# Kernel optimization log

Measured on AMD Instinct MI355X. Metric: run time of the kernel, lower is better.

## Reference

```python
import jax, jax.numpy as jnp
import numpy as np

N = 50000      # nodes
E = 800000     # edges
F = 128        # num_features
H = 128        # hidden_channels
L = 3          # num_layers
P = 32         # num_partitions
EPS = 1e-5     # BatchNorm1d eps


def _batchnorm(h):
    # BatchNorm1d(affine=False, track_running_stats=False): batch stats, biased var
    m = jnp.mean(h, axis=0)
    v = jnp.var(h, axis=0)
    return (h - m) * jax.lax.rsqrt(v + EPS)


def setup_inputs() -> dict:
    key = jax.random.key(0)
    ks = jax.random.split(key, 12)
    x = jax.random.normal(ks[0], (N, F), dtype=jnp.float32)
    edge_index = jax.random.randint(ks[1], (2, E), 0, N)
    edge_weights = jax.random.uniform(ks[2], (E,), dtype=jnp.float32)
    partitions = (jax.random.uniform(ks[3], (N, P)) < (1.0 / P)).astype(jnp.float32)
    node_weights = jax.random.uniform(ks[4], (N,), dtype=jnp.float32)
    edge_curr_node = jax.random.uniform(ks[5], (N,), dtype=jnp.float32)
    conv_w = 0.05 * jax.random.normal(ks[6], (L, F, H), dtype=jnp.float32)
    conv_b = jnp.zeros((L, H), dtype=jnp.float32)
    lin1_w = 0.05 * jax.random.normal(ks[7], (4 * H, H), dtype=jnp.float32)
    lin1_b = jnp.zeros((H,), dtype=jnp.float32)
    lin2_w = 0.05 * jax.random.normal(ks[8], (H, 1), dtype=jnp.float32)
    lin2_b = jnp.zeros((1,), dtype=jnp.float32)
    return {"x": x, "edge_index": edge_index, "edge_weights": edge_weights,
            "partitions": partitions, "node_weights": node_weights,
            "edge_curr_node": edge_curr_node, "conv_w": conv_w, "conv_b": conv_b,
            "lin1_w": lin1_w, "lin1_b": lin1_b, "lin2_w": lin2_w,
            "lin2_b": lin2_b, "curr_node_id": 123}


def reference(x, edge_index, edge_weights, partitions, node_weights,
              edge_curr_node, conv_w, conv_b, lin1_w, lin1_b, lin2_w, lin2_b,
              curr_node_id):
    src, dst = edge_index[0], edge_index[1]
    # GCN normalization with added self-loops (weight 1)
    deg = jax.ops.segment_sum(edge_weights, dst, num_segments=N) + 1.0
    dinv = jax.lax.rsqrt(deg)
    norm = dinv[src] * edge_weights * dinv[dst]          # [E]
    self_norm = (dinv * dinv)[:, None]                   # [N,1]

    h = x
    for l in range(L):
        hw = h @ conv_w[l] + conv_b[l]                   # [N,H]
        agg = jax.ops.segment_sum(hw[src] * norm[:, None], dst, num_segments=N)
        agg = agg + hw * self_norm                       # self-loop term
        h = jax.nn.relu(_batchnorm(agg))

    x_curr = h[curr_node_id]                             # [H]
    # mlp scoring: concat [h | x_curr | edge_col repeated to 2H] -> [N,4H]
    cat = jnp.concatenate([
        h,
        jnp.broadcast_to(x_curr[None, :], (N, H)),
        jnp.broadcast_to(edge_curr_node[:, None], (N, 2 * H)),
    ], axis=1)
    scores = jax.nn.relu(cat @ lin1_w + lin1_b) @ lin2_w + lin2_b  # [N,1]
    # pool == 'sum'
    partition_scores = scores.T @ partitions             # [1,P]
    return (partition_scores, h)
```

## Files before the change

### kernel.cpp

```cpp
#include <hip/hip_runtime.h>

#define N_NODES 50000
#define N_EDGES 800000
#define NP 50048
#define MAXDEG 64
#define PADK 136
#define NCOPY 64
#define EB 3125
#define WPB 512

typedef __bf16 bf16_8 __attribute__((ext_vector_type(8)));
typedef float  f32_4  __attribute__((ext_vector_type(4)));

__device__ inline float2 bf2f2(unsigned int u) {
    union { unsigned int i; float f; } a, b;
    a.i = u << 16;
    b.i = u & 0xffff0000u;
    return make_float2(a.f, b.f);
}

__global__ void k_init_wprep(int* __restrict__ fillp, float* __restrict__ colpart,
                             float* __restrict__ out_head,
                             const float* __restrict__ conv_w, const float* __restrict__ lin1_w,
                             __bf16* __restrict__ WT, float* __restrict__ svec) {
    int b = blockIdx.x;
    if (b < EB) {
        int i = b * 256 + threadIdx.x;
        fillp[i] = 0;
        if (i < 2 * NCOPY * 128) colpart[i] = 0.f;
        if (i < 32) out_head[i] = 0.f;
    } else if (b < EB + WPB) {
        int b2 = b - EB;
        int mat = b2 >> 7, n = b2 & 127, k = threadIdx.x;
        if (k < 128) {
            const float* srcm = (mat < 3) ? (conv_w + (size_t)mat * 16384) : lin1_w;
            WT[((size_t)mat * 128 + n) * 128 + k] = (__bf16)srcm[(size_t)k * 128 + n];
        }
    } else {
        int j = threadIdx.x;
        if (j < 128) {
            float s = 0.f;
            for (int k = 256; k < 512; ++k) s += lin1_w[(size_t)k * 128 + j];
            svec[j] = s;
        }
    }
}

__global__ void k_fillover(const int* __restrict__ src, const int* __restrict__ dst,
                           const float* __restrict__ ew,
                           int* __restrict__ fillp, uint2* __restrict__ esn) {
    int e = blockIdx.x * 256 + threadIdx.x;
    if (e >= N_EDGES) return;
    int d = dst[e];
    int pos = atomicAdd(&fillp[d * 16], 1);
    if (pos < MAXDEG)
        esn[(size_t)d * MAXDEG + pos] = make_uint2((unsigned)src[e], __float_as_uint(ew[e]));
}

__global__ void k_node(const uint2* __restrict__ esn, const int* __restrict__ fillp,
                       float* __restrict__ dinv) {
    int n = blockIdx.x * 256 + threadIdx.x;
    if (n >= N_NODES) return;
    int c = min(fillp[n * 16], MAXDEG);
    float s = 1.0f;
    for (int i = 0; i < c; ++i) s += __uint_as_float(esn[(size_t)n * MAXDEG + i].y);
    dinv[n] = rsqrtf(s);
}

template <int AMODE>
__global__ __launch_bounds__(256) void k_gemm_mfma(const float* __restrict__ A,
                                                   const float* __restrict__ mean,
                                                   const float* __restrict__ rstd,
                                                   const __bf16* __restrict__ WT,
                                                   const float* __restrict__ bias,
                                                   __bf16* __restrict__ C, int nrows) {
    __shared__ __bf16 As[64 * PADK];
    __shared__ __bf16 Ws[128 * PADK];
    int t = threadIdx.x;
    int rowBase = blockIdx.x * 64;
    const uint4* WTg = (const uint4*)WT;
    for (int i = t; i < 2048; i += 256) {
        int n = i >> 4, k8 = i & 15;
        *(uint4*)&Ws[n * PADK + k8 * 8] = WTg[i];
    }
    const float4* A4 = (const float4*)A;
    const float4* M4 = (const float4*)mean;
    const float4* R4 = (const float4*)rstd;
    for (int i = t; i < 1024; i += 256) {
        int r = i >> 4, k8 = i & 15;
        int gr = rowBase + r;
        float4 a0 = make_float4(0.f, 0.f, 0.f, 0.f), a1 = a0;
        if (gr < nrows) {
            a0 = A4[(size_t)gr * 32 + k8 * 2];
            a1 = A4[(size_t)gr * 32 + k8 * 2 + 1];
        }
        if (AMODE == 1) {
            float4 m0 = M4[k8 * 2], m1 = M4[k8 * 2 + 1];
            float4 r0 = R4[k8 * 2], r1 = R4[k8 * 2 + 1];
            a0.x = fmaxf((a0.x - m0.x) * r0.x, 0.f); a0.y = fmaxf((a0.y - m0.y) * r0.y, 0.f);
            a0.z = fmaxf((a0.z - m0.z) * r0.z, 0.f); a0.w = fmaxf((a0.w - m0.w) * r0.w, 0.f);
            a1.x = fmaxf((a1.x - m1.x) * r1.x, 0.f); a1.y = fmaxf((a1.y - m1.y) * r1.y, 0.f);
            a1.z = fmaxf((a1.z - m1.z) * r1.z, 0.f); a1.w = fmaxf((a1.w - m1.w) * r1.w, 0.f);
        }
        bf16_8 o = { (__bf16)a0.x, (__bf16)a0.y, (__bf16)a0.z, (__bf16)a0.w,
                     (__bf16)a1.x, (__bf16)a1.y, (__bf16)a1.z, (__bf16)a1.w };
        *(bf16_8*)&As[r * PADK + k8 * 8] = o;
    }
    __syncthreads();
    int wave = t >> 6, lane = t & 63, quad = lane >> 4, m = lane & 15;
    int ar = wave * 16 + m;
    f32_4 acc[8];
#pragma unroll
    for (int i = 0; i < 8; ++i) acc[i] = (f32_4){0.f, 0.f, 0.f, 0.f};
#pragma unroll
    for (int kk = 0; kk < 4; ++kk) {
        bf16_8 a = *(const bf16_8*)&As[ar * PADK + kk * 32 + quad * 8];
#pragma unroll
        for (int n0 = 0; n0 < 8; ++n0) {
            bf16_8 b = *(const bf16_8*)&Ws[(n0 * 16 + m) * PADK + kk * 32 + quad * 8];
            acc[n0] = __builtin_amdgcn_mfma_f32_16x16x32_bf16(a, b, acc[n0], 0, 0, 0);
        }
    }
    __syncthreads();
#pragma unroll
    for (int n0 = 0; n0 < 8; ++n0) {
        int col = n0 * 16 + m;
        float bi = bias[col];
#pragma unroll
        for (int r = 0; r < 4; ++r) {
            int rr = wave * 16 + quad * 4 + r;
            As[rr * PADK + col] = (__bf16)(acc[n0][r] + bi);
        }
    }
    __syncthreads();
    uint4* Cg = (uint4*)C;
    for (int i = t; i < 1024; i += 256) {
        int r = i >> 4, k8 = i & 15;
        int gr = rowBase + r;
        if (gr < nrows) Cg[(size_t)gr * 16 + k8] = *(const uint4*)&As[r * PADK + k8 * 8];
    }
}

__global__ __launch_bounds__(256) void k_agg(const __bf16* __restrict__ hwb,
                                             const uint2* __restrict__ esn,
                                             const int* __restrict__ fillp,
                                             const float* __restrict__ dinv,
                                             float* __restrict__ agg,
                                             float* __restrict__ colpart) {
    __shared__ float red1[4 * 128], red2[4 * 128];
    int t = threadIdx.x;
    int n = (blockIdx.x * 256 + t) >> 6;
    int lane = t & 63, wave = t >> 6;
    float2 acc = make_float2(0.f, 0.f);
    const unsigned int* hw32 = (const unsigned int*)hwb;
    if (n < N_NODES) {
        float dvn = dinv[n];
        float2 sv = bf2f2(hw32[(size_t)n * 64 + lane]);
        acc.x = sv.x * dvn * dvn; acc.y = sv.y * dvn * dvn;
        int num = min(fillp[n * 16], MAXDEG);
        int s_l = 0; float w_l = 0.f;
        if (lane < num) {
            uint2 e = esn[(size_t)n * MAXDEG + lane];
            s_l = (int)e.x;
            w_l = dinv[s_l] * __uint_as_float(e.y) * dvn;
        }
        int i = 0;
        for (; i + 8 <= num; i += 8) {
            int ss[8]; float ww[8]; unsigned uu[8];
#pragma unroll
            for (int j = 0; j < 8; ++j) { ss[j] = __shfl(s_l, i + j); ww[j] = __shfl(w_l, i + j); }
#pragma unroll
            for (int j = 0; j < 8; ++j) uu[j] = hw32[(size_t)ss[j] * 64 + lane];
#pragma unroll
            for (int j = 0; j < 8; ++j) {
                float2 f = bf2f2(uu[j]);
                acc.x += f.x * ww[j]; acc.y += f.y * ww[j];
            }
        }
        for (; i < num; ++i) {
            int s = __shfl(s_l, i);
            float w = __shfl(w_l, i);
            float2 f = bf2f2(hw32[(size_t)s * 64 + lane]);
            acc.x += f.x * w; acc.y += f.y * w;
        }
        ((float2*)agg)[(size_t)n * 64 + lane] = acc;
    }
    *(float2*)&red1[wave * 128 + 2 * lane] = acc;
    *(float2*)&red2[wave * 128 + 2 * lane] = make_float2(acc.x * acc.x, acc.y * acc.y);
    __syncthreads();
    if (t < 128) {
        float s = red1[t] + red1[128 + t] + red1[256 + t] + red1[384 + t];
        float q = red2[t] + red2[128 + t] + red2[256 + t] + red2[384 + t];
        int c = blockIdx.x & (NCOPY - 1);
        unsafeAtomicAdd(&colpart[c * 128 + t], s);
        unsafeAtomicAdd(&colpart[NCOPY * 128 + c * 128 + t], q);
    }
}

__global__ void k_bnfinal(float* colpart, float* mean, float* rstd) {
    int j = threadIdx.x;
    float s = 0.f, q = 0.f;
    for (int c = 0; c < NCOPY; ++c) {
        s += colpart[c * 128 + j];
        q += colpart[NCOPY * 128 + c * 128 + j];
        colpart[c * 128 + j] = 0.f;
        colpart[NCOPY * 128 + c * 128 + j] = 0.f;
    }
    float m = s * (1.0f / N_NODES);
    float v = q * (1.0f / N_NODES) - m * m;
    mean[j] = m;
    rstd[j] = rsqrtf(v + 1e-5f);
}

__global__ void k_prep(const float* __restrict__ agg, const float* __restrict__ mean,
                       const float* __restrict__ rstd, const int* __restrict__ cid,
                       const float* __restrict__ lin1w, const float* __restrict__ lin1b,
                       float* c0) {
    __shared__ float xc[128];
    int t = threadIdx.x;
    int cn = cid[0];
    float a = agg[(size_t)cn * 128 + t];
    xc[t] = fmaxf((a - mean[t]) * rstd[t], 0.f);
    __syncthreads();
    float acc = lin1b[t];
    for (int k = 0; k < 128; ++k)
        acc += xc[k] * lin1w[(size_t)(128 + k) * 128 + t];
    c0[t] = acc;
}

__global__ __launch_bounds__(256) void k_score_mfma(const float* __restrict__ agg,
                                                    const float* __restrict__ mean,
                                                    const float* __restrict__ rstd,
                                                    const __bf16* __restrict__ WT,
                                                    const float* __restrict__ c0,
                                                    const float* __restrict__ svec,
                                                    const float* __restrict__ ecn,
                                                    const float* __restrict__ lin2w,
                                                    const float* __restrict__ lin2b,
                                                    float* __restrict__ scores,
                                                    float* __restrict__ hout,
                                                    int nrows) {
    __shared__ __bf16 As[64 * PADK];
    __shared__ __bf16 Ws[128 * PADK];
    __shared__ float c0s[128], svs[128], l2s[128];
    int t = threadIdx.x;
    int rowBase = blockIdx.x * 64;
    const uint4* WTg = (const uint4*)WT;
    for (int i = t; i < 2048; i += 256) {
        int n = i >> 4, k8 = i & 15;
        *(uint4*)&Ws[n * PADK + k8 * 8] = WTg[i];
    }
    const float4* A4 = (const float4*)agg;
    const float4* M4 = (const float4*)mean;
    const float4* R4 = (const float4*)rstd;
    float4* H4 = (float4*)hout;
    for (int i = t; i < 1024; i += 256) {
        int r = i >> 4, k8 = i & 15;
        int gr = rowBase + r;
        float4 a0 = make_float4(0.f, 0.f, 0.f, 0.f), a1 = a0;
        if (gr < nrows) {
            a0 = A4[(size_t)gr * 32 + k8 * 2];
            a1 = A4[(size_t)gr * 32 + k8 * 2 + 1];
        }
        float4 m0 = M4[k8 * 2], m1 = M4[k8 * 2 + 1];
        float4 r0 = R4[k8 * 2], r1 = R4[k8 * 2 + 1];
        float4 f0, f1;
        f0.x = fmaxf((a0.x - m0.x) * r0.x, 0.f); f0.y = fmaxf((a0.y - m0.y) * r0.y, 0.f);
        f0.z = fmaxf((a0.z - m0.z) * r0.z, 0.f); f0.w = fmaxf((a0.w - m0.w) * r0.w, 0.f);
        f1.x = fmaxf((a1.x - m1.x) * r1.x, 0.f); f1.y = fmaxf((a1.y - m1.y) * r1.y, 0.f);
        f1.z = fmaxf((a1.z - m1.z) * r1.z, 0.f); f1.w = fmaxf((a1.w - m1.w) * r1.w, 0.f);
        if (gr < nrows) {
            H4[(size_t)gr * 32 + k8 * 2] = f0;
            H4[(size_t)gr * 32 + k8 * 2 + 1] = f1;
        }
        bf16_8 o = { (__bf16)f0.x, (__bf16)f0.y, (__bf16)f0.z, (__bf16)f0.w,
                     (__bf16)f1.x, (__bf16)f1.y, (__bf16)f1.z, (__bf16)f1.w };
        *(bf16_8*)&As[r * PADK + k8 * 8] = o;
    }
    if (t < 128) { c0s[t] = c0[t]; svs[t] = svec[t]; l2s[t] = lin2w[t]; }
    __syncthreads();
    int wave = t >> 6, lane = t & 63, quad = lane >> 4, m = lane & 15;
    int ar = wave * 16 + m;
    f32_4 acc[8];
#pragma unroll
    for (int i = 0; i < 8; ++i) acc[i] = (f32_4){0.f, 0.f, 0.f, 0.f};
#pragma unroll
    for (int kk = 0; kk < 4; ++kk) {
        bf16_8 a = *(const bf16_8*)&As[ar * PADK + kk * 32 + quad * 8];
#pragma unroll
        for (int n0 = 0; n0 < 8; ++n0) {
            bf16_8 b = *(const bf16_8*)&Ws[(n0 * 16 + m) * PADK + kk * 32 + quad * 8];
            acc[n0] = __builtin_amdgcn_mfma_f32_16x16x32_bf16(a, b, acc[n0], 0, 0, 0);
        }
    }
    float l2b = lin2b[0];
#pragma unroll
    for (int r = 0; r < 4; ++r) {
        int row = rowBase + wave * 16 + quad * 4 + r;
        float e = (row < nrows) ? ecn[row] : 0.f;
        float partial = 0.f;
#pragma unroll
        for (int n0 = 0; n0 < 8; ++n0) {
            int col = n0 * 16 + m;
            float v = acc[n0][r] + c0s[col] + e * svs[col];
            partial += fmaxf(v, 0.f) * l2s[col];
        }
        partial += __shfl_xor(partial, 8, 16);
        partial += __shfl_xor(partial, 4, 16);
        partial += __shfl_xor(partial, 2, 16);
        partial += __shfl_xor(partial, 1, 16);
        if (m == 0 && row < nrows) scores[row] = partial + l2b;
    }
}

__global__ void k_partition(const float* __restrict__ scores, const float* __restrict__ part,
                            float* out) {
    __shared__ float red[256];
    int t = threadIdx.x;
    int p = t & 31, rg = t >> 5;
    float acc = 0.f;
    for (int r = blockIdx.x * 8 + rg; r < N_NODES; r += gridDim.x * 8)
        acc += scores[r] * part[(size_t)r * 32 + p];
    red[t] = acc;
    __syncthreads();
    if (t < 32) {
        float s = 0.f;
        for (int i = 0; i < 8; ++i) s += red[i * 32 + t];
        unsafeAtomicAdd(&out[t], s);
    }
}

extern "C" void kernel_launch(void* const* d_in, const int* in_sizes, int n_in,
                              void* d_out, int out_size, void* d_ws, size_t ws_size,
                              hipStream_t stream) {
    const float* x        = (const float*)d_in[0];
    const int*   eidx     = (const int*)d_in[1];
    const float* ew       = (const float*)d_in[2];
    const float* parts    = (const float*)d_in[3];
    const float* ecn      = (const float*)d_in[5];
    const float* conv_w   = (const float*)d_in[6];
    const float* conv_b   = (const float*)d_in[7];
    const float* lin1_w   = (const float*)d_in[8];
    const float* lin1_b   = (const float*)d_in[9];
    const float* lin2_w   = (const float*)d_in[10];
    const float* lin2_b   = (const float*)d_in[11];
    const int*   cid      = (const int*)d_in[12];

    const int* src = eidx;
    const int* dst = eidx + N_EDGES;

    char* p = (char*)d_ws;
    auto alloc = [&](size_t bytes) { char* r = p; p += (bytes + 255) & ~size_t(255); return r; };
    int*    fillp   = (int*)alloc((size_t)N_NODES * 16 * 4);
    uint2*  esn     = (uint2*)alloc((size_t)N_NODES * MAXDEG * 8);
    float*  dinv    = (float*)alloc(NP * 4);
    float*  scores  = (float*)alloc(NP * 4);
    float*  colpart = (float*)alloc(2 * NCOPY * 128 * 4);
    float*  mean    = (float*)alloc(128 * 4);
    float*  rstd    = (float*)alloc(128 * 4);
    float*  c0      = (float*)alloc(128 * 4);
    float*  svec    = (float*)alloc(128 * 4);
    __bf16* WT      = (__bf16*)alloc(4 * 128 * 128 * 2);
    __bf16* hwb     = (__bf16*)alloc((size_t)N_NODES * 128 * 2);
    float*  agg     = (float*)alloc((size_t)N_NODES * 128 * 4);

    float* out_head = (float*)d_out;
    float* hbuf     = (float*)d_out + 32;

    const int NB = (NP + 255) / 256;
    const int GB = (N_NODES + 63) / 64;
    const int AB = (N_NODES * 64 + 255) / 256;

    k_init_wprep<<<EB + WPB + 1, 256, 0, stream>>>(fillp, colpart, out_head,
                                                   conv_w, lin1_w, WT, svec);
    k_fillover<<<EB, 256, 0, stream>>>(src, dst, ew, fillp, esn);
    k_node<<<NB, 256, 0, stream>>>(esn, fillp, dinv);

    for (int l = 0; l < 3; ++l) {
        if (l == 0)
            k_gemm_mfma<0><<<GB, 256, 0, stream>>>(x, mean, rstd, WT, conv_b, hwb, N_NODES);
        else
            k_gemm_mfma<1><<<GB, 256, 0, stream>>>(agg, mean, rstd, WT + (size_t)l * 16384,
                                                   conv_b + (size_t)l * 128, hwb, N_NODES);
        k_agg<<<AB, 256, 0, stream>>>(hwb, esn, fillp, dinv, agg, colpart);
        k_bnfinal<<<1, 128, 0, stream>>>(colpart, mean, rstd);
    }

    k_prep<<<1, 128, 0, stream>>>(agg, mean, rstd, cid, lin1_w, lin1_b, c0);
    k_score_mfma<<<GB, 256, 0, stream>>>(agg, mean, rstd, WT + (size_t)3 * 16384, c0, svec,
                                         ecn, lin2_w, lin2_b, scores, hbuf, N_NODES);
    k_partition<<<256, 256, 0, stream>>>(scores, parts, out_head);
}
```

Measured before the change: 354.2 us.

## Build compact CSR adjacency via bucketed counting sort instead of padded atomic fill

Replaces the padded per-node edge slots (fixed MAXDEG, one global atomic per edge) with a two-level counting sort: a per-block histogram over 64 destination buckets, a scan, a scatter into bucket order, then a per-bucket kernel that builds an exact CSR in shared memory and computes dinv there. The aggregation kernel now reads contiguous CSR ranges, folds dinv[dst] into the stored weight, handles any degree in chunks of 64 rather than truncating at 64, and unrolls the gather by 16. The aim is to cut global atomic contention and the memory footprint of the padded layout, and to improve gather ILP, at the cost of several extra small launches and an extra pass over the edges.

Measured after the change: 460.0 us. +29.9%, slower.

```diff
diff --git a/kernel.cpp b/kernel.cpp
--- a/kernel.cpp
+++ b/kernel.cpp
@@ -3,10 +3,11 @@
 #define N_NODES 50000
 #define N_EDGES 800000
 #define NP 50048
-#define MAXDEG 64
+#define BKT 784
+#define NBKT 64
+#define HB 782
 #define PADK 136
 #define NCOPY 64
-#define EB 3125
 #define WPB 512
 
 typedef __bf16 bf16_8 __attribute__((ext_vector_type(8)));
@@ -19,18 +20,16 @@
     return make_float2(a.f, b.f);
 }
 
-__global__ void k_init_wprep(int* __restrict__ fillp, float* __restrict__ colpart,
-                             float* __restrict__ out_head,
+__global__ void k_init_wprep(float* __restrict__ colpart, float* __restrict__ out_head,
                              const float* __restrict__ conv_w, const float* __restrict__ lin1_w,
                              __bf16* __restrict__ WT, float* __restrict__ svec) {
     int b = blockIdx.x;
-    if (b < EB) {
+    if (b < 64) {
         int i = b * 256 + threadIdx.x;
-        fillp[i] = 0;
-        if (i < 2 * NCOPY * 128) colpart[i] = 0.f;
+        colpart[i] = 0.f;
         if (i < 32) out_head[i] = 0.f;
-    } else if (b < EB + WPB) {
-        int b2 = b - EB;
+    } else if (b < 64 + WPB) {
+        int b2 = b - 64;
         int mat = b2 >> 7, n = b2 & 127, k = threadIdx.x;
         if (k < 128) {
             const float* srcm = (mat < 3) ? (conv_w + (size_t)mat * 16384) : lin1_w;
@@ -46,25 +45,123 @@
     }
 }
 
-__global__ void k_fillover(const int* __restrict__ src, const int* __restrict__ dst,
-                           const float* __restrict__ ew,
-                           int* __restrict__ fillp, uint2* __restrict__ esn) {
-    int e = blockIdx.x * 256 + threadIdx.x;
-    if (e >= N_EDGES) return;
-    int d = dst[e];
-    int pos = atomicAdd(&fillp[d * 16], 1);
-    if (pos < MAXDEG)
-        esn[(size_t)d * MAXDEG + pos] = make_uint2((unsigned)src[e], __float_as_uint(ew[e]));
-}
-
-__global__ void k_node(const uint2* __restrict__ esn, const int* __restrict__ fillp,
-                       float* __restrict__ dinv) {
-    int n = blockIdx.x * 256 + threadIdx.x;
-    if (n >= N_NODES) return;
-    int c = min(fillp[n * 16], MAXDEG);
-    float s = 1.0f;
-    for (int i = 0; i < c; ++i) s += __uint_as_float(esn[(size_t)n * MAXDEG + i].y);
-    dinv[n] = rsqrtf(s);
+__global__ void k_hist(const int* __restrict__ dst, int* __restrict__ counts) {
+    __shared__ int c[NBKT];
+    int t = threadIdx.x, b = blockIdx.x;
+    if (t < NBKT) c[t] = 0;
+    __syncthreads();
+    int e0 = b * 1024;
+    for (int i = t; i < 1024; i += 256) {
+        int e = e0 + i;
+        if (e < N_EDGES) atomicAdd(&c[dst[e] / BKT], 1);
+    }
+    __syncthreads();
+    if (t < NBKT) counts[t * HB + b] = c[t];
+}
+
+__global__ void k_scan(int* __restrict__ counts, int* __restrict__ bucketStart) {
+    __shared__ int p[256];
+    int t = threadIdx.x;
+    int base = t * 196;
+    int sum = 0;
+    for (int i = 0; i < 196; ++i) {
+        int f = base + i;
+        if (f < NBKT * HB) sum += counts[f];
+    }
+    p[t] = sum;
+    __syncthreads();
+    int own = sum;
+    for (int d = 1; d < 256; d <<= 1) {
+        int v = (t >= d) ? p[t - d] : 0;
+        __syncthreads();
+        p[t] += v;
+        __syncthreads();
+    }
+    int run = p[t] - own;
+    for (int i = 0; i < 196; ++i) {
+        int f = base + i;
+        if (f < NBKT * HB) {
+            int v = counts[f];
+            counts[f] = run;
+            if (f % HB == 0) bucketStart[f / HB] = run;
+            run += v;
+        }
+    }
+}
+
+__global__ void k_scatter(const int* __restrict__ src, const int* __restrict__ dst,
+                          const float* __restrict__ ew, const int* __restrict__ counts,
+                          uint2* __restrict__ ebuf) {
+    __shared__ int ofs[NBKT];
+    int t = threadIdx.x, b = blockIdx.x;
+    if (t < NBKT) ofs[t] = counts[t * HB + b];
+    __syncthreads();
+    int e0 = b * 1024;
+    for (int i = t; i < 1024; i += 256) {
+        int e = e0 + i;
+        if (e < N_EDGES) {
+            int d = dst[e];
+            int bkt = d / BKT, dl = d - bkt * BKT;
+            int pos = atomicAdd(&ofs[bkt], 1);
+            ebuf[pos] = make_uint2(((unsigned)dl << 17) | (unsigned)src[e],
+                                   __float_as_uint(ew[e]));
+        }
+    }
+}
+
+__global__ __launch_bounds__(256) void k_build(const uint2* __restrict__ ebuf,
+                                               const int* __restrict__ bucketStart,
+                                               uint2* __restrict__ esn2,
+                                               int* __restrict__ offs, int* __restrict__ cnt,
+                                               float* __restrict__ dinv) {
+    __shared__ int   c784[1024];
+    __shared__ float deg784[1024];
+    __shared__ int   o784[1024];
+    __shared__ int   fill784[1024];
+    __shared__ int   p[256];
+    int b = blockIdx.x, t = threadIdx.x;
+    int base = bucketStart[b];
+    int end  = (b == NBKT - 1) ? N_EDGES : bucketStart[b + 1];
+    for (int i = t; i < 1024; i += 256) { c784[i] = 0; deg784[i] = 1.0f; fill784[i] = 0; }
+    __syncthreads();
+    for (int i = base + t; i < end; i += 256) {
+        uint2 eu = ebuf[i];
+        int dl = eu.x >> 17;
+        atomicAdd(&c784[dl], 1);
+        atomicAdd(&deg784[dl], __uint_as_float(eu.y));
+    }
+    __syncthreads();
+    for (int i = t; i < BKT; i += 256) deg784[i] = rsqrtf(deg784[i]);
+    int s0 = c784[4 * t] + c784[4 * t + 1] + c784[4 * t + 2] + c784[4 * t + 3];
+    p[t] = s0;
+    __syncthreads();
+    int own = s0;
+    for (int d = 1; d < 256; d <<= 1) {
+        int v = (t >= d) ? p[t - d] : 0;
+        __syncthreads();
+        p[t] += v;
+        __syncthreads();
+    }
+    int e0 = p[t] - own;
+    o784[4 * t] = e0;
+    o784[4 * t + 1] = e0 + c784[4 * t];
+    o784[4 * t + 2] = e0 + c784[4 * t] + c784[4 * t + 1];
+    o784[4 * t + 3] = e0 + c784[4 * t] + c784[4 * t + 1] + c784[4 * t + 2];
+    __syncthreads();
+    int nb0 = b * BKT;
+    for (int i = t; i < BKT; i += 256) {
+        int n = nb0 + i;
+        if (n < N_NODES) { offs[n] = base + o784[i]; cnt[n] = c784[i]; dinv[n] = deg784[i]; }
+    }
+    __syncthreads();
+    for (int i = base + t; i < end; i += 256) {
+        uint2 eu = ebuf[i];
+        int dl = eu.x >> 17;
+        int s  = (int)(eu.x & 131071u);
+        int pos = base + o784[dl] + atomicAdd(&fill784[dl], 1);
+        esn2[pos] = make_uint2((unsigned)s,
+                               __float_as_uint(__uint_as_float(eu.y) * deg784[dl]));
+    }
 }
 
 template <int AMODE>
@@ -142,8 +239,9 @@
 }
 
 __global__ __launch_bounds__(256) void k_agg(const __bf16* __restrict__ hwb,
-                                             const uint2* __restrict__ esn,
-                                             const int* __restrict__ fillp,
+                                             const uint2* __restrict__ esn2,
+                                             const int* __restrict__ offs,
+                                             const int* __restrict__ cnt,
                                              const float* __restrict__ dinv,
                                              float* __restrict__ agg,
                                              float* __restrict__ colpart) {
@@ -157,31 +255,47 @@
         float dvn = dinv[n];
         float2 sv = bf2f2(hw32[(size_t)n * 64 + lane]);
         acc.x = sv.x * dvn * dvn; acc.y = sv.y * dvn * dvn;
-        int num = min(fillp[n * 16], MAXDEG);
-        int s_l = 0; float w_l = 0.f;
-        if (lane < num) {
-            uint2 e = esn[(size_t)n * MAXDEG + lane];
-            s_l = (int)e.x;
-            w_l = dinv[s_l] * __uint_as_float(e.y) * dvn;
-        }
-        int i = 0;
-        for (; i + 8 <= num; i += 8) {
-            int ss[8]; float ww[8]; unsigned uu[8];
-#pragma unroll
-            for (int j = 0; j < 8; ++j) { ss[j] = __shfl(s_l, i + j); ww[j] = __shfl(w_l, i + j); }
-#pragma unroll
-            for (int j = 0; j < 8; ++j) uu[j] = hw32[(size_t)ss[j] * 64 + lane];
-#pragma unroll
-            for (int j = 0; j < 8; ++j) {
-                float2 f = bf2f2(uu[j]);
-                acc.x += f.x * ww[j]; acc.y += f.y * ww[j];
+        int beg = offs[n], num = cnt[n];
+        for (int c0 = 0; c0 < num; c0 += 64) {
+            int nn = min(64, num - c0);
+            int s_l = 0; float w_l = 0.f;
+            if (lane < nn) {
+                uint2 e = esn2[beg + c0 + lane];
+                s_l = (int)e.x;
+                w_l = dinv[s_l] * __uint_as_float(e.y);
             }
-        }
-        for (; i < num; ++i) {
-            int s = __shfl(s_l, i);
-            float w = __shfl(w_l, i);
-            float2 f = bf2f2(hw32[(size_t)s * 64 + lane]);
-            acc.x += f.x * w; acc.y += f.y * w;
+            int i = 0;
+            for (; i + 16 <= nn; i += 16) {
+                int ss[16]; float ww[16]; unsigned uu[16];
+#pragma unroll
+                for (int j = 0; j < 16; ++j) { ss[j] = __shfl(s_l, i + j); ww[j] = __shfl(w_l, i + j); }
+#pragma unroll
+                for (int j = 0; j < 16; ++j) uu[j] = hw32[(size_t)ss[j] * 64 + lane];
+#pragma unroll
+                for (int j = 0; j < 16; ++j) {
+                    float2 f = bf2f2(uu[j]);
+                    acc.x += f.x * ww[j]; acc.y += f.y * ww[j];
+                }
+            }
+            for (; i + 4 <= nn; i += 4) {
+                int s0 = __shfl(s_l, i),     s1 = __shfl(s_l, i + 1);
+                int s2 = __shfl(s_l, i + 2), s3 = __shfl(s_l, i + 3);
+                float w0 = __shfl(w_l, i),     w1 = __shfl(w_l, i + 1);
+                float w2 = __shfl(w_l, i + 2), w3 = __shfl(w_l, i + 3);
+                unsigned u0 = hw32[(size_t)s0 * 64 + lane];
+                unsigned u1 = hw32[(size_t)s1 * 64 + lane];
+                unsigned u2 = hw32[(size_t)s2 * 64 + lane];
+                unsigned u3 = hw32[(size_t)s3 * 64 + lane];
+                float2 f0 = bf2f2(u0), f1 = bf2f2(u1), f2 = bf2f2(u2), f3 = bf2f2(u3);
+                acc.x += f0.x * w0 + f1.x * w1 + f2.x * w2 + f3.x * w3;
+                acc.y += f0.y * w0 + f1.y * w1 + f2.y * w2 + f3.y * w3;
+            }
+            for (; i < nn; ++i) {
+                int s = __shfl(s_l, i);
+                float w = __shfl(w_l, i);
+                float2 f = bf2f2(hw32[(size_t)s * 64 + lane]);
+                acc.x += f.x * w; acc.y += f.y * w;
+            }
         }
         ((float2*)agg)[(size_t)n * 64 + lane] = acc;
     }
@@ -351,8 +465,12 @@
 
     char* p = (char*)d_ws;
     auto alloc = [&](size_t bytes) { char* r = p; p += (bytes + 255) & ~size_t(255); return r; };
-    int*    fillp   = (int*)alloc((size_t)N_NODES * 16 * 4);
-    uint2*  esn     = (uint2*)alloc((size_t)N_NODES * MAXDEG * 8);
+    int*    counts  = (int*)alloc((size_t)NBKT * HB * 4);
+    int*    bstart  = (int*)alloc(NBKT * 4);
+    uint2*  ebuf    = (uint2*)alloc((size_t)N_EDGES * 8);
+    uint2*  esn2    = (uint2*)alloc((size_t)N_EDGES * 8);
+    int*    offs    = (int*)alloc(NP * 4);
+    int*    cnt     = (int*)alloc(NP * 4);
     float*  dinv    = (float*)alloc(NP * 4);
     float*  scores  = (float*)alloc(NP * 4);
     float*  colpart = (float*)alloc(2 * NCOPY * 128 * 4);
@@ -367,14 +485,14 @@
     float* out_head = (float*)d_out;
     float* hbuf     = (float*)d_out + 32;
 
-    const int NB = (NP + 255) / 256;
     const int GB = (N_NODES + 63) / 64;
     const int AB = (N_NODES * 64 + 255) / 256;
 
-    k_init_wprep<<<EB + WPB + 1, 256, 0, stream>>>(fillp, colpart, out_head,
-                                                   conv_w, lin1_w, WT, svec);
-    k_fillover<<<EB, 256, 0, stream>>>(src, dst, ew, fillp, esn);
-    k_node<<<NB, 256, 0, stream>>>(esn, fillp, dinv);
+    k_init_wprep<<<64 + WPB + 1, 256, 0, stream>>>(colpart, out_head, conv_w, lin1_w, WT, svec);
+    k_hist<<<HB, 256, 0, stream>>>(dst, counts);
+    k_scan<<<1, 256, 0, stream>>>(counts, bstart);
+    k_scatter<<<HB, 256, 0, stream>>>(src, dst, ew, counts, ebuf);
+    k_build<<<NBKT, 256, 0, stream>>>(ebuf, bstart, esn2, offs, cnt, dinv);
 
     for (int l = 0; l < 3; ++l) {
         if (l == 0)
@@ -382,7 +500,7 @@
         else
             k_gemm_mfma<1><<<GB, 256, 0, stream>>>(agg, mean, rstd, WT + (size_t)l * 16384,
                                                    conv_b + (size_t)l * 128, hwb, N_NODES);
-        k_agg<<<AB, 256, 0, stream>>>(hwb, esn, fillp, dinv, agg, colpart);
+        k_agg<<<AB, 256, 0, stream>>>(hwb, esn2, offs, cnt, dinv, agg, colpart);
         k_bnfinal<<<1, 128, 0, stream>>>(colpart, mean, rstd);
     }
 
```
